# Performance work log

Hardware: AMD Instinct MI355X
Metric: run time of the kernel (lower is better)

## Reference

```python
import jax, jax.numpy as jnp
import numpy as np

DIM = 512
PDIM = 64
NUM_HEAD = 8
HEAD_DIM = DIM // NUM_HEAD
SCALE = HEAD_DIM ** -0.5
EPS = 1e-6


def setup_inputs() -> dict:
    key = jax.random.key(0)
    ks = jax.random.split(key, 8)
    B, N = 8, 2048
    x_token = jax.random.normal(ks[0], (B, N, DIM), dtype=jnp.float32)
    x_path = jax.random.normal(ks[1], (B, N, PDIM), dtype=jnp.float32)
    idx_cluster = jax.random.randint(ks[2], (B, N), 0, 16, dtype=jnp.int32)
    # weights stored as [in, out] (y = x @ W + b), matching torch Linear math
    Wqk = jax.random.normal(ks[3], (DIM, 2 * DIM), dtype=jnp.float32) * 0.02
    Wv = jax.random.normal(ks[4], (DIM, DIM), dtype=jnp.float32) * 0.02
    Wpv = jax.random.normal(ks[5], (PDIM, PDIM), dtype=jnp.float32) * 0.02
    Wproj = jax.random.normal(ks[6], (DIM, DIM), dtype=jnp.float32) * 0.02
    bproj = jax.random.normal(ks[7], (DIM,), dtype=jnp.float32) * 0.02
    return {"x_token": x_token, "x_path": x_path, "idx_cluster": idx_cluster,
            "cluster_num": 16, "Wqk": Wqk, "Wv": Wv, "Wpv": Wpv,
            "Wproj": Wproj, "bproj": bproj}


def reference(x_token, x_path, idx_cluster, cluster_num, Wqk, Wv, Wpv, Wproj, bproj):
    B, N, C = x_token.shape
    qk = x_token @ Wqk                      # [B,N,2C]
    q, k = qk[..., :C], qk[..., C:]
    v = x_token @ Wv                        # [B,N,C]
    pv = x_path @ Wpv                       # dead code in original; kept for fidelity

    idx_shuffle = jnp.argsort(idx_cluster, axis=1)          # [B,N]
    idx_restore = jnp.argsort(idx_shuffle, axis=1)

    v_s = jnp.take_along_axis(v, idx_shuffle[..., None], axis=1)
    pv_s = jnp.take_along_axis(pv, idx_shuffle[..., None], axis=1)  # unused (faithful)

    attn_map = jnp.einsum('bic,bjc->bij', q, k) * SCALE     # [B,N,N]

    # torch does two gathers, both with dim=1; the second index is constant along
    # rows, so attn2[b,i,j] = attn_map[b, idx_shuffle[b, idx_shuffle[b,j]], j]
    double = jnp.take_along_axis(idx_shuffle, idx_shuffle, axis=1)  # [B,N]
    col_vals = jnp.take_along_axis(jnp.swapaxes(attn_map, 1, 2), double[..., None], axis=2)[..., 0]  # [B,N]
    attn = jnp.broadcast_to(col_vals[:, None, :], (B, N, N))

    # contiguous per-cluster block mask in sorted order == equality of sorted ids
    s = jnp.sort(idx_cluster, axis=1)
    mask = (s[:, :, None] == s[:, None, :]) & (s[:, :, None] < cluster_num)

    attn = jnp.where(mask, attn, jnp.float32(-1e9))
    attn = jnp.exp(attn.astype(jnp.float32))
    attn = (attn + EPS / N) / (jnp.sum(attn, axis=-1, keepdims=True) + EPS)

    out = attn @ v_s                                         # [B,N,C]
    out = jnp.swapaxes(out, 1, 2).reshape(B, N, C)           # faithful layout scramble
    out = jnp.take_along_axis(out, idx_restore[..., None], axis=1)
    x_out = out @ Wproj + bproj
    return x_out, attn_map
```

## Files before the change

### kernel.cpp

```cpp
#include <hip/hip_runtime.h>
#include <hip/hip_bf16.h>

typedef __attribute__((ext_vector_type(8))) short short8;
typedef __attribute__((ext_vector_type(4))) float floatx4;

__device__ __forceinline__ unsigned short f2bfu(float f) {
    unsigned u = __float_as_uint(f);
    unsigned rounding = 0x7fffu + ((u >> 16) & 1u);
    return (unsigned short)((u + rounding) >> 16);
}
__device__ __forceinline__ float bfu2f(unsigned short u) {
    return __uint_as_float(((unsigned)u) << 16);
}

__device__ __forceinline__ void async_ld16(const void* g, void* l) {
    __builtin_amdgcn_global_load_lds(
        (const __attribute__((address_space(1))) void*)g,
        (__attribute__((address_space(3))) void*)l, 16, 0, 0);
}

#define B_  8
#define N_  2048
#define C_  512
#define NC_ 16
#define SL_ 8

__global__ __launch_bounds__(256) void cvt_x(const float4* __restrict__ x,
                                             unsigned short* __restrict__ xbf) {
    size_t i = (size_t)blockIdx.x * 256 + threadIdx.x;
    float4 f = x[i];
    unsigned short u0 = f2bfu(f.x), u1 = f2bfu(f.y), u2 = f2bfu(f.z), u3 = f2bfu(f.w);
    uint2 p;
    p.x = (unsigned)u0 | ((unsigned)u1 << 16);
    p.y = (unsigned)u2 | ((unsigned)u3 << 16);
    *(uint2*)(xbf + 4 * i) = p;
}

__global__ __launch_bounds__(256) void cvt_wqk(const float* __restrict__ Wqk,
                                               unsigned short* __restrict__ WT) {
    int id = blockIdx.x * 256 + threadIdx.x;
    int n = id >> 9, k = id & 511;
    WT[id] = f2bfu(Wqk[(size_t)k * 1024 + n]);
}

__global__ __launch_bounds__(256) void sort_kernel(const int* __restrict__ idx_cluster,
                                                   int* __restrict__ shuf,
                                                   int* __restrict__ restore,
                                                   int* __restrict__ svals,
                                                   int* __restrict__ dbl,
                                                   int* __restrict__ cstart) {
    int b = blockIdx.x, t = threadIdx.x;
    __shared__ int vals[N_];
    __shared__ int seghist[256 * 17];
    __shared__ int cbase[NC_], ctot[NC_];
    __shared__ int shufs[N_];
    const int* src = idx_cluster + (size_t)b * N_;
    for (int j = t; j < N_; j += 256) vals[j] = src[j];
    for (int c = 0; c < NC_; ++c) seghist[t * 17 + c] = 0;
    __syncthreads();
    for (int i = 0; i < 8; ++i) {
        int c = vals[t * 8 + i];
        seghist[t * 17 + c]++;
    }
    __syncthreads();
    if (t < NC_) {
        int run = 0;
        for (int s = 0; s < 256; ++s) {
            int x = seghist[s * 17 + t];
            seghist[s * 17 + t] = run;
            run += x;
        }
        ctot[t] = run;
    }
    __syncthreads();
    if (t == 0) {
        int run = 0;
        for (int c = 0; c < NC_; ++c) {
            cbase[c] = run;
            cstart[b * 17 + c] = run;
            run += ctot[c];
        }
        cstart[b * 17 + NC_] = run;
    }
    __syncthreads();
    for (int i = 0; i < 8; ++i) {
        int p = t * 8 + i;
        int c = vals[p];
        int pos = cbase[c] + seghist[t * 17 + c];
        seghist[t * 17 + c]++;
        shufs[pos] = p;
    }
    __syncthreads();
    for (int j = t; j < N_; j += 256) {
        int sj = shufs[j];
        shuf[(size_t)b * N_ + j] = sj;
        svals[(size_t)b * N_ + j] = vals[sj];
        restore[(size_t)b * N_ + sj] = j;
        dbl[(size_t)b * N_ + j] = shufs[sj];
    }
}

template <int MODE>
__global__ __launch_bounds__(256) void gemm_bt(const unsigned short* __restrict__ A,
                                               const unsigned short* __restrict__ Bt,
                                               float* __restrict__ outF,
                                               unsigned short* __restrict__ outQ,
                                               unsigned short* __restrict__ outK) {
    constexpr int K = 512;
    int t = threadIdx.x;
    int lane = t & 63, wave = t >> 6;
    int wm = (wave & 1) * 64, wn = (wave >> 1) * 64;
    int m0 = blockIdx.y * 128, n0 = blockIdx.x * 128;
    if (MODE == 1) {
        size_t b = blockIdx.z;
        A += b * (size_t)N_ * 512;
        Bt += b * (size_t)N_ * 512;
        outF += b * (size_t)N_ * N_;
    }
    __shared__ __align__(16) unsigned short As[128 * 64];
    __shared__ __align__(16) unsigned short Bs[128 * 64];
    floatx4 acc[4][4] = {};
    int l15 = lane & 15, q4 = lane >> 4;
    int srow = lane >> 3, schk = lane & 7;
    int sgc = schk ^ srow;
    int xr = l15 & 7;

    for (int k0 = 0; k0 < K; k0 += 64) {
        __syncthreads();
#pragma unroll
        for (int i = 0; i < 4; ++i) {
            int cid = i * 4 + wave;
            int row = cid * 8 + srow;
            async_ld16(A + (size_t)(m0 + row) * 512 + k0 + sgc * 8, (char*)As + cid * 1024);
            async_ld16(Bt + (size_t)(n0 + row) * 512 + k0 + sgc * 8, (char*)Bs + cid * 1024);
        }
        __syncthreads();
#pragma unroll
        for (int kk = 0; kk < 2; ++kk) {
            int csw = (((kk * 4 + q4) ^ xr) * 8);
            short8 af[4], bfr[4];
#pragma unroll
            for (int mi = 0; mi < 4; ++mi)
                af[mi] = *(const short8*)(&As[(wm + mi * 16 + l15) * 64 + csw]);
#pragma unroll
            for (int ni = 0; ni < 4; ++ni)
                bfr[ni] = *(const short8*)(&Bs[(wn + ni * 16 + l15) * 64 + csw]);
#pragma unroll
            for (int mi = 0; mi < 4; ++mi)
#pragma unroll
                for (int ni = 0; ni < 4; ++ni)
                    acc[mi][ni] = __builtin_amdgcn_mfma_f32_16x16x32_bf16(af[mi], bfr[ni], acc[mi][ni], 0, 0, 0);
        }
    }
#pragma unroll
    for (int mi = 0; mi < 4; ++mi) {
#pragma unroll
        for (int ni = 0; ni < 4; ++ni) {
#pragma unroll
            for (int r = 0; r < 4; ++r) {
                int row = m0 + wm + mi * 16 + q4 * 4 + r;
                int col = n0 + wn + ni * 16 + l15;
                float v = acc[mi][ni][r];
                if (MODE == 0) {
                    unsigned short u = f2bfu(v);
                    if (col < 512) outQ[(size_t)row * 512 + col] = u;
                    else           outK[(size_t)row * 512 + col - 512] = u;
                } else {
                    outF[(size_t)row * N_ + col] = v * 0.125f;
                }
            }
        }
    }
}

__global__ __launch_bounds__(256) void cluster_reduce2(const float* __restrict__ attn,
                                                       const int* __restrict__ shuf,
                                                       const int* __restrict__ dbl,
                                                       const int* __restrict__ cstart,
                                                       const unsigned short* __restrict__ xbf,
                                                       float* __restrict__ xepart,
                                                       float* __restrict__ Spart) {
    int c = blockIdx.x, b = blockIdx.y, sl = blockIdx.z, t = threadIdx.x;
    int start = cstart[b * 17 + c], end = cstart[b * 17 + c + 1];
    int n = end - start;
    int i0 = (n * sl) / SL_, i1 = (n * (sl + 1)) / SL_;
    int cnt = i1 - i0;
    __shared__ float e_lds[256];
    __shared__ int row_lds[256];
    if (t < cnt) {
        int j = start + i0 + t;
        int dj = dbl[(size_t)b * N_ + j];
        float e = expf(attn[(size_t)b * N_ * N_ + (size_t)dj * N_ + j]);
        e_lds[t] = e;
        row_lds[t] = shuf[(size_t)b * N_ + j];
    }
    __syncthreads();
    if (t == 0) {
        float s = 0.f;
        for (int i = 0; i < cnt; ++i) s += e_lds[i];
        Spart[(b * SL_ + sl) * NC_ + c] = s;
    }
    float a0 = 0.f, a1 = 0.f;
    for (int i = 0; i < cnt; ++i) {
        float e = e_lds[i];
        unsigned u = *(const unsigned*)(xbf + ((size_t)b * N_ + row_lds[i]) * 512 + 2 * t);
        a0 += e * bfu2f((unsigned short)u);
        a1 += e * bfu2f((unsigned short)(u >> 16));
    }
    float2 o; o.x = a0; o.y = a1;
    *(float2*)(xepart + (((size_t)(b * SL_ + sl) * NC_ + c) * 512 + 2 * t)) = o;
}

__global__ __launch_bounds__(256) void combine_xe(const float* __restrict__ xepart,
                                                  const float* __restrict__ Spart,
                                                  float* __restrict__ xe,
                                                  float* __restrict__ Stot) {
    int c = blockIdx.x, b = blockIdx.y, t = threadIdx.x;
    float a0 = 0.f, a1 = 0.f;
    for (int sl = 0; sl < SL_; ++sl) {
        float2 o = *(const float2*)(xepart + (((size_t)(b * SL_ + sl) * NC_ + c) * 512 + 2 * t));
        a0 += o.x; a1 += o.y;
    }
    float2 r; r.x = a0; r.y = a1;
    *(float2*)(xe + ((size_t)b * NC_ + c) * 512 + 2 * t) = r;
    if (t == 0) {
        float S = 0.f;
        for (int sl = 0; sl < SL_; ++sl) S += Spart[(b * SL_ + sl) * NC_ + c];
        Stot[b * NC_ + c] = S;
    }
}

__global__ __launch_bounds__(256) void ovw_kernel(const float* __restrict__ xe,
                                                  const float* __restrict__ Stot,
                                                  const float* __restrict__ Wv,
                                                  float* __restrict__ Ot) {
    int c = blockIdx.x, b = blockIdx.y, t = threadIdx.x;
    __shared__ float xl[512];
    for (int i = t; i < 512; i += 256) xl[i] = xe[((size_t)b * NC_ + c) * 512 + i];
    __syncthreads();
    float S = Stot[b * NC_ + c];
    float inv = S > 0.f ? 1.f / S : 0.f;
    float a0 = 0.f, a1 = 0.f;
    for (int k = 0; k < 512; ++k) {
        float xv = xl[k];
        float2 w = *(const float2*)(Wv + (size_t)k * 512 + 2 * t);
        a0 += xv * w.x; a1 += xv * w.y;
    }
    Ot[((size_t)b * 512 + 2 * t) * NC_ + c] = a0 * inv;
    Ot[((size_t)b * 512 + 2 * t + 1) * NC_ + c] = a1 * inv;
}

__global__ __launch_bounds__(256) void build_wg(const float* __restrict__ Wproj,
                                                const int* __restrict__ cstart,
                                                unsigned int* __restrict__ Wg) {
    int c = blockIdx.x;
    int bg = blockIdx.y;
    int b = bg >> 2, g = bg & 3;
    int t = threadIdx.x;
    int lo = cstart[b * 17 + c] - g * 512;
    int hi = cstart[b * 17 + c + 1] - g * 512;
    lo = lo < 0 ? 0 : lo;
    hi = hi > 512 ? 512 : hi;
    float a0 = 0.f, a1 = 0.f;
    for (int cd = lo; cd < hi; ++cd) {
        float2 w = *(const float2*)(Wproj + (size_t)cd * 512 + 2 * t);
        a0 += w.x; a1 += w.y;
    }
    Wg[(size_t)bg * NC_ * 256 + c * 256 + t] =
        (unsigned)f2bfu(a0) | ((unsigned)f2bfu(a1) << 16);
}

__global__ __launch_bounds__(256) void xout_kernel(const float* __restrict__ Ot,
                                                   const unsigned int* __restrict__ Wg,
                                                   const int* __restrict__ restore,
                                                   const float* __restrict__ bias,
                                                   float* __restrict__ xout) {
    int nb = blockIdx.x, b = blockIdx.y, t = threadIdx.x;
    int n0 = nb * 64;
    __shared__ int r_lds[64];
    if (t < 64) r_lds[t] = restore[(size_t)b * N_ + n0 + t];
    __syncthreads();
    float b0 = bias[2 * t], b1 = bias[2 * t + 1];
    const float* Otb = Ot + (size_t)b * 512 * NC_;
    for (int g = 0; g < 4; ++g) {
        const unsigned int* wg = Wg + (size_t)(b * 4 + g) * NC_ * 256 + t;
        float wx[NC_], wy[NC_];
#pragma unroll
        for (int c = 0; c < NC_; ++c) {
            unsigned u = wg[c * 256];
            wx[c] = bfu2f((unsigned short)u);
            wy[c] = bfu2f((unsigned short)(u >> 16));
        }
        for (int i = 0; i < 64; ++i) {
            int r = r_lds[i];
            if ((r & 3) != g) continue;
            int rq = r >> 2;
            const float4* op = (const float4*)(Otb + rq * NC_);
            float o[NC_];
            *(float4*)&o[0]  = op[0];
            *(float4*)&o[4]  = op[1];
            *(float4*)&o[8]  = op[2];
            *(float4*)&o[12] = op[3];
            float a0 = b0, a1 = b1;
#pragma unroll
            for (int c = 0; c < NC_; ++c) { a0 += o[c] * wx[c]; a1 += o[c] * wy[c]; }
            float2 res; res.x = a0; res.y = a1;
            *(float2*)(xout + ((size_t)b * N_ + n0 + i) * 512 + 2 * t) = res;
        }
    }
}

extern "C" void kernel_launch(void* const* d_in, const int* in_sizes, int n_in,
                              void* d_out, int out_size, void* d_ws, size_t ws_size,
                              hipStream_t stream) {
    const float* x_token = (const float*)d_in[0];
    const int* idx_cluster = (const int*)d_in[2];
    const float* Wqk = (const float*)d_in[4];
    const float* Wv = (const float*)d_in[5];
    const float* Wproj = (const float*)d_in[7];
    const float* bproj = (const float*)d_in[8];

    float* x_out = (float*)d_out;
    float* attn = x_out + (size_t)B_ * N_ * C_;

    char* ws = (char*)d_ws;
    size_t off = 0;
    auto alloc = [&](size_t bytes) {
        void* p = ws + off;
        off += (bytes + 255) & ~(size_t)255;
        return p;
    };
    unsigned short* WqkT = (unsigned short*)alloc(1024 * 512 * 2);
    unsigned short* xbf = (unsigned short*)alloc((size_t)B_ * N_ * C_ * 2);
    unsigned short* qbf = (unsigned short*)alloc((size_t)B_ * N_ * C_ * 2);
    unsigned short* kbf = (unsigned short*)alloc((size_t)B_ * N_ * C_ * 2);
    int* shuf = (int*)alloc((size_t)B_ * N_ * 4);
    int* restore = (int*)alloc((size_t)B_ * N_ * 4);
    int* svals = (int*)alloc((size_t)B_ * N_ * 4);
    int* dbl = (int*)alloc((size_t)B_ * N_ * 4);
    int* cstart = (int*)alloc(B_ * 17 * 4);
    float* Ot = (float*)alloc((size_t)B_ * 512 * NC_ * 4);
    float* xepart = (float*)alloc((size_t)B_ * SL_ * NC_ * 512 * 4);
    float* Spart = (float*)alloc((size_t)B_ * SL_ * NC_ * 4);
    float* xe = (float*)alloc((size_t)B_ * NC_ * 512 * 4);
    float* Stot = (float*)alloc((size_t)B_ * NC_ * 4);
    unsigned int* Wg = (unsigned int*)alloc((size_t)B_ * 4 * NC_ * 256 * 4);

    cvt_x<<<dim3((B_ * N_ * C_) / (256 * 4)), dim3(256), 0, stream>>>((const float4*)x_token, xbf);
    cvt_wqk<<<dim3((1024 * 512) / 256), dim3(256), 0, stream>>>(Wqk, WqkT);

    sort_kernel<<<dim3(B_), dim3(256), 0, stream>>>(idx_cluster, shuf, restore, svals, dbl, cstart);

    build_wg<<<dim3(NC_, B_ * 4), dim3(256), 0, stream>>>(Wproj, cstart, Wg);

    gemm_bt<0><<<dim3(1024 / 128, 16384 / 128, 1), dim3(256), 0, stream>>>(
        xbf, WqkT, nullptr, qbf, kbf);

    gemm_bt<1><<<dim3(N_ / 128, N_ / 128, B_), dim3(256), 0, stream>>>(
        qbf, kbf, attn, nullptr, nullptr);

    cluster_reduce2<<<dim3(NC_, B_, SL_), dim3(256), 0, stream>>>(
        attn, shuf, dbl, cstart, xbf, xepart, Spart);

    combine_xe<<<dim3(NC_, B_), dim3(256), 0, stream>>>(xepart, Spart, xe, Stot);

    ovw_kernel<<<dim3(NC_, B_), dim3(256), 0, stream>>>(xe, Stot, Wv, Ot);

    xout_kernel<<<dim3(N_ / 64, B_), dim3(256), 0, stream>>>(Ot, Wg, restore, bproj, x_out);
}
```

Before: 390.1 us.

## Refactor QK^T as x·(Wq Wk^T)·x^T and fuse exp gather into attention GEMM

Replaces the separate Q and K projections with a single precomputed 512x512 matrix M = Wq·Wk^T, so only xM is computed and the attention GEMM uses xM against x directly. The large projection GEMM output width drops from 1024 to 512. The attention GEMM epilogue also captures exp of the needed diagonal-gathered entries into a small evals buffer, so cluster_reduce no longer re-reads attn. The x and weight conversions are merged into one launch, and combine_xe is folded into ovw_kernel. Forming M in bf16 and reusing bf16 x as the K operand changes rounding relative to the reference.

```diff
diff --git a/kernel.cpp b/kernel.cpp
--- a/kernel.cpp
+++ b/kernel.cpp
@@ -25,22 +25,25 @@
 #define NC_ 16
 #define SL_ 8
 
-__global__ __launch_bounds__(256) void cvt_x(const float4* __restrict__ x,
-                                             unsigned short* __restrict__ xbf) {
-    size_t i = (size_t)blockIdx.x * 256 + threadIdx.x;
-    float4 f = x[i];
-    unsigned short u0 = f2bfu(f.x), u1 = f2bfu(f.y), u2 = f2bfu(f.z), u3 = f2bfu(f.w);
-    uint2 p;
-    p.x = (unsigned)u0 | ((unsigned)u1 << 16);
-    p.y = (unsigned)u2 | ((unsigned)u3 << 16);
-    *(uint2*)(xbf + 4 * i) = p;
-}
-
-__global__ __launch_bounds__(256) void cvt_wqk(const float* __restrict__ Wqk,
-                                               unsigned short* __restrict__ WT) {
-    int id = blockIdx.x * 256 + threadIdx.x;
-    int n = id >> 9, k = id & 511;
-    WT[id] = f2bfu(Wqk[(size_t)k * 1024 + n]);
+__global__ __launch_bounds__(256) void cvt_all(const float4* __restrict__ x,
+                                               const float* __restrict__ Wqk,
+                                               unsigned short* __restrict__ xbf,
+                                               unsigned short* __restrict__ Wq_bf,
+                                               unsigned short* __restrict__ Wk_bf) {
+    int bx = blockIdx.x, t = threadIdx.x;
+    if (bx < 8192) {
+        size_t i = (size_t)bx * 256 + t;
+        float4 f = x[i];
+        uint2 p;
+        p.x = (unsigned)f2bfu(f.x) | ((unsigned)f2bfu(f.y) << 16);
+        p.y = (unsigned)f2bfu(f.z) | ((unsigned)f2bfu(f.w) << 16);
+        *(uint2*)(xbf + 4 * i) = p;
+    } else {
+        int id = (bx - 8192) * 256 + t;
+        int r = id >> 9, c = id & 511;
+        Wq_bf[id] = f2bfu(Wqk[(size_t)r * 1024 + c]);
+        Wk_bf[id] = f2bfu(Wqk[(size_t)r * 1024 + 512 + c]);
+    }
 }
 
 __global__ __launch_bounds__(256) void sort_kernel(const int* __restrict__ idx_cluster,
@@ -104,21 +107,25 @@
 __global__ __launch_bounds__(256) void gemm_bt(const unsigned short* __restrict__ A,
                                                const unsigned short* __restrict__ Bt,
                                                float* __restrict__ outF,
-                                               unsigned short* __restrict__ outQ,
-                                               unsigned short* __restrict__ outK) {
+                                               unsigned short* __restrict__ outB,
+                                               const int* __restrict__ dbl,
+                                               float* __restrict__ evals) {
     constexpr int K = 512;
     int t = threadIdx.x;
     int lane = t & 63, wave = t >> 6;
     int wm = (wave & 1) * 64, wn = (wave >> 1) * 64;
     int m0 = blockIdx.y * 128, n0 = blockIdx.x * 128;
+    size_t b = 0;
     if (MODE == 1) {
-        size_t b = blockIdx.z;
+        b = blockIdx.z;
         A += b * (size_t)N_ * 512;
         Bt += b * (size_t)N_ * 512;
         outF += b * (size_t)N_ * N_;
     }
     __shared__ __align__(16) unsigned short As[128 * 64];
     __shared__ __align__(16) unsigned short Bs[128 * 64];
+    __shared__ int dbl_lds[MODE == 1 ? 128 : 1];
+    if (MODE == 1 && t < 128) dbl_lds[t] = dbl[b * N_ + n0 + t];
     floatx4 acc[4][4] = {};
     int l15 = lane & 15, q4 = lane >> 4;
     int srow = lane >> 3, schk = lane & 7;
@@ -156,26 +163,27 @@
     for (int mi = 0; mi < 4; ++mi) {
 #pragma unroll
         for (int ni = 0; ni < 4; ++ni) {
+            int colL = wn + ni * 16 + l15;
+            int dj = (MODE == 1) ? dbl_lds[colL] : 0;
 #pragma unroll
             for (int r = 0; r < 4; ++r) {
-                int row = m0 + wm + mi * 16 + q4 * 4 + r;
-                int col = n0 + wn + ni * 16 + l15;
+                int rowL = wm + mi * 16 + q4 * 4 + r;
                 float v = acc[mi][ni][r];
                 if (MODE == 0) {
-                    unsigned short u = f2bfu(v);
-                    if (col < 512) outQ[(size_t)row * 512 + col] = u;
-                    else           outK[(size_t)row * 512 + col - 512] = u;
+                    outB[(size_t)(m0 + rowL) * 512 + n0 + colL] = f2bfu(v);
                 } else {
-                    outF[(size_t)row * N_ + col] = v * 0.125f;
+                    float av = v * 0.125f;
+                    outF[(size_t)(m0 + rowL) * N_ + n0 + colL] = av;
+                    if (dj == m0 + rowL)
+                        evals[b * N_ + n0 + colL] = expf(av);
                 }
             }
         }
     }
 }
 
-__global__ __launch_bounds__(256) void cluster_reduce2(const float* __restrict__ attn,
+__global__ __launch_bounds__(256) void cluster_reduce2(const float* __restrict__ evals,
                                                        const int* __restrict__ shuf,
-                                                       const int* __restrict__ dbl,
                                                        const int* __restrict__ cstart,
                                                        const unsigned short* __restrict__ xbf,
                                                        float* __restrict__ xepart,
@@ -189,9 +197,7 @@
     __shared__ int row_lds[256];
     if (t < cnt) {
         int j = start + i0 + t;
-        int dj = dbl[(size_t)b * N_ + j];
-        float e = expf(attn[(size_t)b * N_ * N_ + (size_t)dj * N_ + j]);
-        e_lds[t] = e;
+        e_lds[t] = evals[(size_t)b * N_ + j];
         row_lds[t] = shuf[(size_t)b * N_ + j];
     }
     __syncthreads();
@@ -211,34 +217,23 @@
     *(float2*)(xepart + (((size_t)(b * SL_ + sl) * NC_ + c) * 512 + 2 * t)) = o;
 }
 
-__global__ __launch_bounds__(256) void combine_xe(const float* __restrict__ xepart,
+__global__ __launch_bounds__(256) void ovw_kernel(const float* __restrict__ xepart,
                                                   const float* __restrict__ Spart,
-                                                  float* __restrict__ xe,
-                                                  float* __restrict__ Stot) {
-    int c = blockIdx.x, b = blockIdx.y, t = threadIdx.x;
-    float a0 = 0.f, a1 = 0.f;
-    for (int sl = 0; sl < SL_; ++sl) {
-        float2 o = *(const float2*)(xepart + (((size_t)(b * SL_ + sl) * NC_ + c) * 512 + 2 * t));
-        a0 += o.x; a1 += o.y;
-    }
-    float2 r; r.x = a0; r.y = a1;
-    *(float2*)(xe + ((size_t)b * NC_ + c) * 512 + 2 * t) = r;
-    if (t == 0) {
-        float S = 0.f;
-        for (int sl = 0; sl < SL_; ++sl) S += Spart[(b * SL_ + sl) * NC_ + c];
-        Stot[b * NC_ + c] = S;
-    }
-}
-
-__global__ __launch_bounds__(256) void ovw_kernel(const float* __restrict__ xe,
-                                                  const float* __restrict__ Stot,
                                                   const float* __restrict__ Wv,
                                                   float* __restrict__ Ot) {
     int c = blockIdx.x, b = blockIdx.y, t = threadIdx.x;
     __shared__ float xl[512];
-    for (int i = t; i < 512; i += 256) xl[i] = xe[((size_t)b * NC_ + c) * 512 + i];
-    __syncthreads();
-    float S = Stot[b * NC_ + c];
+    for (int i = t; i < 512; i += 256) {
+        float s = 0.f;
+#pragma unroll
+        for (int sl = 0; sl < SL_; ++sl)
+            s += xepart[(((size_t)(b * SL_ + sl) * NC_ + c) * 512 + i)];
+        xl[i] = s;
+    }
+    __syncthreads();
+    float S = 0.f;
+#pragma unroll
+    for (int sl = 0; sl < SL_; ++sl) S += Spart[(b * SL_ + sl) * NC_ + c];
     float inv = S > 0.f ? 1.f / S : 0.f;
     float a0 = 0.f, a1 = 0.f;
     for (int k = 0; k < 512; ++k) {
@@ -330,41 +325,42 @@
         off += (bytes + 255) & ~(size_t)255;
         return p;
     };
-    unsigned short* WqkT = (unsigned short*)alloc(1024 * 512 * 2);
+    unsigned short* Wq_bf = (unsigned short*)alloc(512 * 512 * 2);
+    unsigned short* Wk_bf = (unsigned short*)alloc(512 * 512 * 2);
+    unsigned short* MT_bf = (unsigned short*)alloc(512 * 512 * 2);
     unsigned short* xbf = (unsigned short*)alloc((size_t)B_ * N_ * C_ * 2);
-    unsigned short* qbf = (unsigned short*)alloc((size_t)B_ * N_ * C_ * 2);
-    unsigned short* kbf = (unsigned short*)alloc((size_t)B_ * N_ * C_ * 2);
+    unsigned short* xMbf = (unsigned short*)alloc((size_t)B_ * N_ * C_ * 2);
     int* shuf = (int*)alloc((size_t)B_ * N_ * 4);
     int* restore = (int*)alloc((size_t)B_ * N_ * 4);
     int* svals = (int*)alloc((size_t)B_ * N_ * 4);
     int* dbl = (int*)alloc((size_t)B_ * N_ * 4);
     int* cstart = (int*)alloc(B_ * 17 * 4);
+    float* evals = (float*)alloc((size_t)B_ * N_ * 4);
     float* Ot = (float*)alloc((size_t)B_ * 512 * NC_ * 4);
     float* xepart = (float*)alloc((size_t)B_ * SL_ * NC_ * 512 * 4);
     float* Spart = (float*)alloc((size_t)B_ * SL_ * NC_ * 4);
-    float* xe = (float*)alloc((size_t)B_ * NC_ * 512 * 4);
-    float* Stot = (float*)alloc((size_t)B_ * NC_ * 4);
     unsigned int* Wg = (unsigned int*)alloc((size_t)B_ * 4 * NC_ * 256 * 4);
 
-    cvt_x<<<dim3((B_ * N_ * C_) / (256 * 4)), dim3(256), 0, stream>>>((const float4*)x_token, xbf);
-    cvt_wqk<<<dim3((1024 * 512) / 256), dim3(256), 0, stream>>>(Wqk, WqkT);
+    cvt_all<<<dim3(8192 + 1024), dim3(256), 0, stream>>>(
+        (const float4*)x_token, Wqk, xbf, Wq_bf, Wk_bf);
 
     sort_kernel<<<dim3(B_), dim3(256), 0, stream>>>(idx_cluster, shuf, restore, svals, dbl, cstart);
 
     build_wg<<<dim3(NC_, B_ * 4), dim3(256), 0, stream>>>(Wproj, cstart, Wg);
 
-    gemm_bt<0><<<dim3(1024 / 128, 16384 / 128, 1), dim3(256), 0, stream>>>(
-        xbf, WqkT, nullptr, qbf, kbf);
+    gemm_bt<0><<<dim3(512 / 128, 512 / 128, 1), dim3(256), 0, stream>>>(
+        Wk_bf, Wq_bf, nullptr, MT_bf, nullptr, nullptr);
+
+    gemm_bt<0><<<dim3(512 / 128, 16384 / 128, 1), dim3(256), 0, stream>>>(
+        xbf, MT_bf, nullptr, xMbf, nullptr, nullptr);
 
     gemm_bt<1><<<dim3(N_ / 128, N_ / 128, B_), dim3(256), 0, stream>>>(
-        qbf, kbf, attn, nullptr, nullptr);
+        xMbf, xbf, attn, nullptr, dbl, evals);
 
     cluster_reduce2<<<dim3(NC_, B_, SL_), dim3(256), 0, stream>>>(
-        attn, shuf, dbl, cstart, xbf, xepart, Spart);
-
-    combine_xe<<<dim3(NC_, B_), dim3(256), 0, stream>>>(xepart, Spart, xe, Stot);
-
-    ovw_kernel<<<dim3(NC_, B_), dim3(256), 0, stream>>>(xe, Stot, Wv, Ot);
+        evals, shuf, cstart, xbf, xepart, Spart);
+
+    ovw_kernel<<<dim3(NC_, B_), dim3(256), 0, stream>>>(xepart, Spart, Wv, Ot);
 
     xout_kernel<<<dim3(N_ / 64, B_), dim3(256), 0, stream>>>(Ot, Wg, restore, bproj, x_out);
 }
```

Measured after the change: 388.2 us. No clear change (-0.5%).
